# Kernel tuning notes

Measured on AMD Instinct MI355X. Metric: run time of the kernel, lower is better.

Reference implementation:

```python
import jax, jax.numpy as jnp
import numpy as np

B_SZ = 4; L = 2048; IN_DIM = 32; D_MODEL = 256; N_LAYERS = 2
ED = 512; N_STATE = 16; DT_RANK = 16; D_CONV = 4


def setup_inputs() -> dict:
    key = jax.random.key(0)
    ks = jax.random.split(key, 12)
    def rn(k, shape, scale=0.02):
        return jax.random.normal(k, shape, jnp.float32) * scale
    return {
        "x": jax.random.normal(ks[0], (B_SZ, L, IN_DIM), jnp.float32),
        "enc_w": rn(ks[1], (D_MODEL, IN_DIM), 0.1),
        "enc_b": jnp.zeros((D_MODEL,), jnp.float32),
        "norm_w": jnp.ones((N_LAYERS, D_MODEL), jnp.float32),
        "in_proj_w": rn(ks[2], (N_LAYERS, 2 * ED, D_MODEL)),
        "conv_w": rn(ks[3], (N_LAYERS, ED, D_CONV), 0.1),
        "conv_b": jnp.zeros((N_LAYERS, ED), jnp.float32),
        "x_proj_w": rn(ks[4], (N_LAYERS, DT_RANK + 2 * N_STATE, ED)),
        "dt_proj_w": rn(ks[5], (N_LAYERS, ED, DT_RANK), 0.1),
        "dt_proj_b": rn(ks[6], (N_LAYERS, ED), 0.5),
        # S4D-real init: A_log[l, e, n] = log(n+1)
        "A_log": jnp.log(jnp.tile(jnp.arange(1, N_STATE + 1, dtype=jnp.float32), (N_LAYERS, ED, 1))),
        "D_param": jnp.ones((N_LAYERS, ED), jnp.float32),
        "out_proj_w": rn(ks[7], (N_LAYERS, D_MODEL, ED)),
        "dec_w": rn(ks[8], (1, D_MODEL), 0.1),
        "dec_b": jnp.zeros((1,), jnp.float32),
    }


def _rmsnorm(x, w, eps=1e-5):
    return x * jax.lax.rsqrt(jnp.mean(x * x, axis=-1, keepdims=True) + eps) * w


def _silu(x):
    return x * jax.nn.sigmoid(x)


def _selective_scan(x, delta, A, Bm, Cm, Dp):
    # x, delta: (B, L, ED); A: (ED, N); Bm, Cm: (B, L, N); Dp: (ED,)
    def step(h, t):
        d_t, b_t, c_t, x_t = t  # (B,ED) (B,N) (B,N) (B,ED)
        dA = jnp.exp(d_t[..., None] * A)               # (B, ED, N)
        h = dA * h + (d_t * x_t)[..., None] * b_t[:, None, :]
        y = jnp.einsum('ben,bn->be', h, c_t)
        return h, y
    h0 = jnp.zeros((x.shape[0], A.shape[0], A.shape[1]), x.dtype)
    xs = (jnp.swapaxes(delta, 0, 1), jnp.swapaxes(Bm, 0, 1),
          jnp.swapaxes(Cm, 0, 1), jnp.swapaxes(x, 0, 1))
    _, ys = jax.lax.scan(step, h0, xs)                 # ys: (L, B, ED)
    return jnp.swapaxes(ys, 0, 1) + Dp * x


def _mamba_block(x, p):
    xz = jnp.einsum('bld,ed->ble', x, p['in_proj_w'])  # (B, L, 2*ED)
    xb, z = jnp.split(xz, 2, axis=-1)
    # causal depthwise conv over time
    xc = jnp.swapaxes(xb, 1, 2)                        # (B, ED, L)
    kern = p['conv_w'][:, None, :]                     # (ED, 1, K)
    xc = jax.lax.conv_general_dilated(xc, kern, (1,), [(D_CONV - 1, 0)],
                                      feature_group_count=ED)
    xb = _silu(jnp.swapaxes(xc, 1, 2) + p['conv_b'])
    dbc = jnp.einsum('ble,fe->blf', xb, p['x_proj_w'])
    dt, Bm, Cm = jnp.split(dbc, [DT_RANK, DT_RANK + N_STATE], axis=-1)
    delta = jax.nn.softplus(jnp.einsum('blr,er->ble', dt, p['dt_proj_w']) + p['dt_proj_b'])
    A = -jnp.exp(p['A_log'])
    y = _selective_scan(xb, delta, A, Bm, Cm, p['D_param'])
    y = y * _silu(z)
    return jnp.einsum('ble,de->bld', y, p['out_proj_w'])


def reference(x, enc_w, enc_b, norm_w, in_proj_w, conv_w, conv_b, x_proj_w,
              dt_proj_w, dt_proj_b, A_log, D_param, out_proj_w, dec_w, dec_b):
    h = jnp.einsum('bli,di->bld', x, enc_w) + enc_b
    for l in range(N_LAYERS):
        p = {'in_proj_w': in_proj_w[l], 'conv_w': conv_w[l], 'conv_b': conv_b[l],
             'x_proj_w': x_proj_w[l], 'dt_proj_w': dt_proj_w[l], 'dt_proj_b': dt_proj_b[l],
             'A_log': A_log[l], 'D_param': D_param[l], 'out_proj_w': out_proj_w[l]}
        h = h + _mamba_block(_rmsnorm(h, norm_w[l]), p)
    out = jax.nn.sigmoid(jnp.einsum('bld,od->blo', h, dec_w) + dec_b)
    return out[:, -1, 0]
```

## Files before the change

kernel.cpp:

```cpp
#include <hip/hip_runtime.h>
#include <math.h>

#define BSZ 4
#define SEQ 2048
#define INDIM 32
#define DM 256
#define ED 512
#define NST 16
#define DTR 16
#define MROWS (BSZ * SEQ)
#define CH 64
#define LC (SEQ / CH)

typedef unsigned short u16;
typedef unsigned int u32;
typedef __bf16 bf16x8 __attribute__((ext_vector_type(8)));
typedef float f32x4 __attribute__((ext_vector_type(4)));

__device__ __forceinline__ float silu_f(float x) { return x / (1.f + __expf(-x)); }

__device__ __forceinline__ u16 f2bf(float x) {
  union { float f; unsigned u; } c; c.f = x;
  return (u16)((c.u + 0x7FFF + ((c.u >> 16) & 1)) >> 16);
}
__device__ __forceinline__ float bf2f(u16 v) {
  union { unsigned u; float f; } c; c.u = ((unsigned)v) << 16;
  return c.f;
}
__device__ __forceinline__ u32 pack2(float lo, float hi) {
  return (u32)f2bf(lo) | ((u32)f2bf(hi) << 16);
}

template <bool ACCUM>
__global__ __launch_bounds__(256) void gemm_bf16_f32(const u16* __restrict__ A,
                                                     const u16* __restrict__ B,
                                                     float* __restrict__ C,
                                                     int M, int N, int K,
                                                     int lda, int ldc) {
  __shared__ u16 As[128][40];
  __shared__ u16 Bs[128][40];
  const int tid = threadIdx.x;
  const int m0 = blockIdx.y * 128;
  const int n0 = blockIdx.x * 128;
  const int wid = tid >> 6;
  const int lane = tid & 63;
  const int wm = (wid >> 1) * 64, wn = (wid & 1) * 64;
  const int l15 = lane & 15, l4 = lane >> 4;
  const int arow = tid >> 1;
  const int ak = (tid & 1) * 16;
  f32x4 acc[4][4];
  const f32x4 zero = {0.f, 0.f, 0.f, 0.f};
#pragma unroll
  for (int i = 0; i < 4; i++)
#pragma unroll
    for (int j = 0; j < 4; j++) acc[i][j] = zero;

  for (int k0 = 0; k0 < K; k0 += 32) {
    const u16* ap = A + (size_t)(m0 + arow) * lda + k0 + ak;
    *(int4*)&As[arow][ak]     = *(const int4*)(ap);
    *(int4*)&As[arow][ak + 8] = *(const int4*)(ap + 8);
    int4 bv0 = {0, 0, 0, 0}, bv1 = {0, 0, 0, 0};
    if (n0 + arow < N) {
      const u16* bp = B + (size_t)(n0 + arow) * K + k0 + ak;
      bv0 = *(const int4*)(bp);
      bv1 = *(const int4*)(bp + 8);
    }
    *(int4*)&Bs[arow][ak]     = bv0;
    *(int4*)&Bs[arow][ak + 8] = bv1;
    __syncthreads();
    bf16x8 af[4], bfr[4];
#pragma unroll
    for (int i = 0; i < 4; i++) {
      af[i]  = *(const bf16x8*)&As[wm + i * 16 + l15][l4 * 8];
      bfr[i] = *(const bf16x8*)&Bs[wn + i * 16 + l15][l4 * 8];
    }
#pragma unroll
    for (int i = 0; i < 4; i++)
#pragma unroll
      for (int j = 0; j < 4; j++)
        acc[i][j] = __builtin_amdgcn_mfma_f32_16x16x32_bf16(af[i], bfr[j], acc[i][j], 0, 0, 0);
    __syncthreads();
  }
#pragma unroll
  for (int i = 0; i < 4; i++) {
    const int mb = m0 + wm + i * 16 + l4 * 4;
#pragma unroll
    for (int j = 0; j < 4; j++) {
      const int n = n0 + wn + j * 16 + l15;
      if (n < N) {
        float* p = C + (size_t)mb * ldc + n;
#pragma unroll
        for (int r = 0; r < 4; r++) {
          float v = acc[i][j][r];
          if (ACCUM) v += p[(size_t)r * ldc];
          p[(size_t)r * ldc] = v;
        }
      }
    }
  }
}

__global__ __launch_bounds__(256) void gemm_bf16_u16(const u16* __restrict__ A,
                                                     const u16* __restrict__ B,
                                                     u16* __restrict__ C,
                                                     int M, int N, int K,
                                                     int lda, int ldc) {
  __shared__ u16 As[128][40];
  __shared__ u16 Bs[128][40];
  const int tid = threadIdx.x;
  const int m0 = blockIdx.y * 128;
  const int n0 = blockIdx.x * 128;
  const int wid = tid >> 6;
  const int lane = tid & 63;
  const int wm = (wid >> 1) * 64, wn = (wid & 1) * 64;
  const int l15 = lane & 15, l4 = lane >> 4;
  const int arow = tid >> 1;
  const int ak = (tid & 1) * 16;
  f32x4 acc[4][4];
  const f32x4 zero = {0.f, 0.f, 0.f, 0.f};
#pragma unroll
  for (int i = 0; i < 4; i++)
#pragma unroll
    for (int j = 0; j < 4; j++) acc[i][j] = zero;

  for (int k0 = 0; k0 < K; k0 += 32) {
    const u16* ap = A + (size_t)(m0 + arow) * lda + k0 + ak;
    *(int4*)&As[arow][ak]     = *(const int4*)(ap);
    *(int4*)&As[arow][ak + 8] = *(const int4*)(ap + 8);
    const u16* bp = B + (size_t)(n0 + arow) * K + k0 + ak;
    *(int4*)&Bs[arow][ak]     = *(const int4*)(bp);
    *(int4*)&Bs[arow][ak + 8] = *(const int4*)(bp + 8);
    __syncthreads();
    bf16x8 af[4], bfr[4];
#pragma unroll
    for (int i = 0; i < 4; i++) {
      af[i]  = *(const bf16x8*)&As[wm + i * 16 + l15][l4 * 8];
      bfr[i] = *(const bf16x8*)&Bs[wn + i * 16 + l15][l4 * 8];
    }
#pragma unroll
    for (int i = 0; i < 4; i++)
#pragma unroll
      for (int j = 0; j < 4; j++)
        acc[i][j] = __builtin_amdgcn_mfma_f32_16x16x32_bf16(af[i], bfr[j], acc[i][j], 0, 0, 0);
    __syncthreads();
  }
#pragma unroll
  for (int i = 0; i < 4; i++) {
    const int mb = m0 + wm + i * 16 + l4 * 4;
#pragma unroll
    for (int j = 0; j < 4; j++) {
      const int n = n0 + wn + j * 16 + l15;
      u16* p = C + (size_t)mb * ldc + n;
#pragma unroll
      for (int r = 0; r < 4; r++) p[(size_t)r * ldc] = f2bf(acc[i][j][r]);
    }
  }
}

__global__ __launch_bounds__(256) void gemm_nt_enc(const float* __restrict__ A,
                                                   const float* __restrict__ B,
                                                   const float* __restrict__ bias,
                                                   float* __restrict__ C,
                                                   int M, int N, int K, int lda) {
  __shared__ float As[16][65];
  __shared__ float Bs[16][65];
  const int tid = threadIdx.x;
  const int m0 = blockIdx.y * 64;
  const int n0 = blockIdx.x * 64;
  const int tm = tid & 15, tn = tid >> 4;
  const int lrow = tid >> 2;
  const int lk = (tid & 3) << 2;
  float acc[4][4] = {};
  for (int k0 = 0; k0 < K; k0 += 16) {
    {
      const float4 a = *(const float4*)(A + (size_t)(m0 + lrow) * lda + k0 + lk);
      As[lk + 0][lrow] = a.x; As[lk + 1][lrow] = a.y;
      As[lk + 2][lrow] = a.z; As[lk + 3][lrow] = a.w;
    }
    {
      float4 b = make_float4(0.f, 0.f, 0.f, 0.f);
      if (n0 + lrow < N) b = *(const float4*)(B + (size_t)(n0 + lrow) * K + k0 + lk);
      Bs[lk + 0][lrow] = b.x; Bs[lk + 1][lrow] = b.y;
      Bs[lk + 2][lrow] = b.z; Bs[lk + 3][lrow] = b.w;
    }
    __syncthreads();
#pragma unroll
    for (int k = 0; k < 16; k++) {
      float a4[4], b4[4];
#pragma unroll
      for (int i = 0; i < 4; i++) a4[i] = As[k][tm * 4 + i];
#pragma unroll
      for (int j = 0; j < 4; j++) b4[j] = Bs[k][tn * 4 + j];
#pragma unroll
      for (int i = 0; i < 4; i++)
#pragma unroll
        for (int j = 0; j < 4; j++) acc[i][j] = fmaf(a4[i], b4[j], acc[i][j]);
    }
    __syncthreads();
  }
#pragma unroll
  for (int i = 0; i < 4; i++) {
    const int m = m0 + tm * 4 + i;
#pragma unroll
    for (int j = 0; j < 4; j++) {
      const int n = n0 + tn * 4 + j;
      if (n < N) C[(size_t)m * N + n] = acc[i][j] + bias[n];
    }
  }
}

#define S_IN (2 * 1024 * 256)
#define S_OUT (2 * 256 * 512)
#define S_XP (2 * 48 * 512)
__global__ __launch_bounds__(256) void cvt_weights_k(const float* __restrict__ w1,
                                                     const float* __restrict__ w2,
                                                     const float* __restrict__ w3,
                                                     u16* __restrict__ o1,
                                                     u16* __restrict__ o2,
                                                     u16* __restrict__ o3) {
  const int i = blockIdx.x * 256 + threadIdx.x;
  if (i < S_IN) o1[i] = f2bf(w1[i]);
  else if (i < S_IN + S_OUT) o2[i - S_IN] = f2bf(w2[i - S_IN]);
  else if (i < S_IN + S_OUT + S_XP) o3[i - S_IN - S_OUT] = f2bf(w3[i - S_IN - S_OUT]);
}

__global__ __launch_bounds__(256) void rmsnorm_k(const float* __restrict__ h,
                                                 const float* __restrict__ w,
                                                 u16* __restrict__ out16) {
  __shared__ float sh[4];
  __shared__ float sscale;
  const int row = blockIdx.x;
  const int tid = threadIdx.x;
  const float v = h[(size_t)row * DM + tid];
  float s = v * v;
#pragma unroll
  for (int off = 32; off; off >>= 1) s += __shfl_xor(s, off, 64);
  if ((tid & 63) == 0) sh[tid >> 6] = s;
  __syncthreads();
  if (tid == 0) {
    float t = sh[0] + sh[1] + sh[2] + sh[3];
    sscale = rsqrtf(t * (1.0f / DM) + 1e-5f);
  }
  __syncthreads();
  out16[(size_t)row * DM + tid] = f2bf(v * sscale * w[tid]);
}

__global__ __launch_bounds__(256) void conv_silu_k(const u16* __restrict__ xz16,
                                                   const float* __restrict__ cw,
                                                   const float* __restrict__ cb,
                                                   u16* __restrict__ out16) {
  const int idx = blockIdx.x * 256 + threadIdx.x;
  const int e = idx & (ED - 1);
  const int row = idx >> 9;
  const int t = row & (SEQ - 1);
  const float4 w = *(const float4*)(cw + e * 4);
  const u16* col = xz16 + e;
  float acc = cb[e];
  const float v0 = (t >= 3) ? bf2f(col[(size_t)(row - 3) * 1024]) : 0.f;
  const float v1 = (t >= 2) ? bf2f(col[(size_t)(row - 2) * 1024]) : 0.f;
  const float v2 = (t >= 1) ? bf2f(col[(size_t)(row - 1) * 1024]) : 0.f;
  const float v3 = bf2f(col[(size_t)row * 1024]);
  acc += v0 * w.x + v1 * w.y + v2 * w.z + v3 * w.w;
  out16[idx] = f2bf(silu_f(acc));
}

__global__ __launch_bounds__(256) void dt_softplus_k(const float* __restrict__ dbc,
                                                     const float* __restrict__ dtw,
                                                     const float* __restrict__ dtb,
                                                     const u16* __restrict__ xbc16,
                                                     u32* __restrict__ pairs) {
  __shared__ float sdt[DTR];
  const int row = blockIdx.y;
  const int e = blockIdx.x * 256 + threadIdx.x;
  if (threadIdx.x < DTR) sdt[threadIdx.x] = dbc[(size_t)row * 48 + threadIdx.x];
  __syncthreads();
  const float* w = dtw + (size_t)e * DTR;
  float s = dtb[e];
#pragma unroll
  for (int r = 0; r < DTR; r++) s = fmaf(sdt[r], w[r], s);
  const float sp = fmaxf(s, 0.f) + log1pf(__expf(-fabsf(s)));
  const float xv = bf2f(xbc16[(size_t)row * ED + e]);
  pairs[(size_t)row * ED + e] = pack2(sp, sp * xv);
}

__global__ __launch_bounds__(256) void scan_pass1(const u32* __restrict__ pairs,
                                                  const float* __restrict__ dbc,
                                                  u16* __restrict__ hend16,
                                                  float* __restrict__ Sbuf,
                                                  const float* __restrict__ A_log) {
  __shared__ float sB[LC][16];
  const int tid = threadIdx.x;
  const int e = blockIdx.x * 256 + tid;
  const int c = blockIdx.y;
  const int b = blockIdx.z;
  const int row0 = b * SEQ + c * LC;
  float Aen[16];
  {
    const float4* ap = (const float4*)(A_log + (size_t)e * 16);
#pragma unroll
    for (int q = 0; q < 4; q++) {
      float4 v = ap[q];
      Aen[4 * q + 0] = -__expf(v.x); Aen[4 * q + 1] = -__expf(v.y);
      Aen[4 * q + 2] = -__expf(v.z); Aen[4 * q + 3] = -__expf(v.w);
    }
  }
  for (int idx = tid; idx < LC * 16; idx += 256)
    sB[idx >> 4][idx & 15] = dbc[(size_t)(row0 + (idx >> 4)) * 48 + DTR + (idx & 15)];
  __syncthreads();
  const u32* pp = pairs + (size_t)row0 * ED + e;
  float h[16];
#pragma unroll
  for (int n = 0; n < 16; n++) h[n] = 0.f;
  float S = 0.f;
  u32 p = pp[0];
  for (int t = 0; t < LC; t++) {
    const u32 pn = (t + 1 < LC) ? pp[(size_t)(t + 1) * ED] : p;
    const float d = bf2f((u16)(p & 0xffff));
    const float dx = bf2f((u16)(p >> 16));
    S += d;
    const float4* bp = (const float4*)sB[t];
    const float4 B0 = bp[0], B1 = bp[1], B2 = bp[2], B3 = bp[3];
    const float Bv[16] = {B0.x, B0.y, B0.z, B0.w, B1.x, B1.y, B1.z, B1.w,
                          B2.x, B2.y, B2.z, B2.w, B3.x, B3.y, B3.z, B3.w};
#pragma unroll
    for (int n = 0; n < 16; n++) h[n] = __expf(d * Aen[n]) * h[n] + dx * Bv[n];
    p = pn;
  }
  u32 wbuf[8];
#pragma unroll
  for (int q = 0; q < 8; q++) wbuf[q] = pack2(h[2 * q], h[2 * q + 1]);
  u16* hp = hend16 + ((size_t)(c * BSZ + b) * ED + e) * 16;
  *(int4*)(hp) = *(int4*)&wbuf[0];
  *(int4*)(hp + 8) = *(int4*)&wbuf[4];
  Sbuf[(size_t)(c * BSZ + b) * ED + e] = S;
}

__global__ __launch_bounds__(256) void scan_mid(u16* __restrict__ hend16,
                                                const float* __restrict__ Sbuf,
                                                const float* __restrict__ A_log) {
  const int idx = blockIdx.x * 256 + threadIdx.x;
  const int en = idx & 8191;
  const int b = idx >> 13;
  const int e = en >> 4;
  const float A = -__expf(A_log[en]);
  float h = 0.f;
#pragma unroll 4
  for (int c = 0; c < CH; c++) {
    const size_t base = (size_t)(c * BSZ + b) * 8192 + en;
    const float he = bf2f(hend16[base]);
    const float Sv = Sbuf[(size_t)(c * BSZ + b) * ED + e];
    hend16[base] = f2bf(h);
    h = __expf(A * Sv) * h + he;
  }
}

__global__ __launch_bounds__(256) void scan_pass2(const u32* __restrict__ pairs,
                                                  const u16* __restrict__ xbc16,
                                                  const float* __restrict__ dbc,
                                                  u16* __restrict__ xz16,
                                                  const u16* __restrict__ hin16,
                                                  const float* __restrict__ A_log,
                                                  const float* __restrict__ Dp) {
  __shared__ float sB[LC][16];
  __shared__ float sC[LC][16];
  const int tid = threadIdx.x;
  const int e = blockIdx.x * 256 + tid;
  const int c = blockIdx.y;
  const int b = blockIdx.z;
  const int row0 = b * SEQ + c * LC;
  float Aen[16];
  {
    const float4* ap = (const float4*)(A_log + (size_t)e * 16);
#pragma unroll
    for (int q = 0; q < 4; q++) {
      float4 v = ap[q];
      Aen[4 * q + 0] = -__expf(v.x); Aen[4 * q + 1] = -__expf(v.y);
      Aen[4 * q + 2] = -__expf(v.z); Aen[4 * q + 3] = -__expf(v.w);
    }
  }
  for (int idx = tid; idx < LC * 32; idx += 256) {
    const int i = idx >> 5, jj = idx & 31;
    const float v = dbc[(size_t)(row0 + i) * 48 + DTR + jj];
    if (jj < 16) sB[i][jj] = v; else sC[i][jj - 16] = v;
  }
  __syncthreads();
  float h[16];
  {
    const u16* hp = hin16 + ((size_t)(c * BSZ + b) * ED + e) * 16;
    int4 v0 = *(const int4*)(hp);
    int4 v1 = *(const int4*)(hp + 8);
    const u32* wv = (const u32*)&v0;
    const u32* wv1 = (const u32*)&v1;
#pragma unroll
    for (int q = 0; q < 4; q++) {
      h[2 * q] = bf2f((u16)(wv[q] & 0xffff));
      h[2 * q + 1] = bf2f((u16)(wv[q] >> 16));
      h[8 + 2 * q] = bf2f((u16)(wv1[q] & 0xffff));
      h[8 + 2 * q + 1] = bf2f((u16)(wv1[q] >> 16));
    }
  }
  const float De = Dp[e];
  const u32* pp = pairs + (size_t)row0 * ED + e;
  const u16* xp = xbc16 + (size_t)row0 * ED + e;
  const u16* zp = xz16 + (size_t)row0 * 1024 + ED + e;
  u16* yw = xz16 + (size_t)row0 * 1024 + e;
  u32 p = pp[0];
  float xv = bf2f(xp[0]);
  float zv = bf2f(zp[0]);
  for (int t = 0; t < LC; t++) {
    const int tn = (t + 1 < LC) ? t + 1 : t;
    const u32 pn = pp[(size_t)tn * ED];
    const float xnx = bf2f(xp[(size_t)tn * ED]);
    const float znx = bf2f(zp[(size_t)tn * 1024]);
    const float d = bf2f((u16)(p & 0xffff));
    const float dx = bf2f((u16)(p >> 16));
    const float4* bp = (const float4*)sB[t];
    const float4 B0 = bp[0], B1 = bp[1], B2 = bp[2], B3 = bp[3];
    const float Bv[16] = {B0.x, B0.y, B0.z, B0.w, B1.x, B1.y, B1.z, B1.w,
                          B2.x, B2.y, B2.z, B2.w, B3.x, B3.y, B3.z, B3.w};
    const float4* cp = (const float4*)sC[t];
    const float4 C0 = cp[0], C1 = cp[1], C2 = cp[2], C3 = cp[3];
    const float Cv[16] = {C0.x, C0.y, C0.z, C0.w, C1.x, C1.y, C1.z, C1.w,
                          C2.x, C2.y, C2.z, C2.w, C3.x, C3.y, C3.z, C3.w};
    float y0 = 0.f, y1 = 0.f, y2 = 0.f, y3 = 0.f;
#pragma unroll
    for (int n = 0; n < 16; n++) {
      h[n] = __expf(d * Aen[n]) * h[n] + dx * Bv[n];
      if ((n & 3) == 0) y0 = fmaf(h[n], Cv[n], y0);
      else if ((n & 3) == 1) y1 = fmaf(h[n], Cv[n], y1);
      else if ((n & 3) == 2) y2 = fmaf(h[n], Cv[n], y2);
      else y3 = fmaf(h[n], Cv[n], y3);
    }
    float y = ((y0 + y1) + (y2 + y3)) + De * xv;
    y *= silu_f(zv);
    yw[(size_t)t * 1024] = f2bf(y);
    p = pn; xv = xnx; zv = znx;
  }
}

__global__ __launch_bounds__(64) void decode_k(const float* __restrict__ h,
                                               const float* __restrict__ dw,
                                               const float* __restrict__ db,
                                               float* __restrict__ out) {
  const int b = blockIdx.x;
  const int tid = threadIdx.x;
  const float* row = h + ((size_t)b * SEQ + SEQ - 1) * DM;
  float s = 0.f;
  for (int i = tid; i < DM; i += 64) s = fmaf(row[i], dw[i], s);
#pragma unroll
  for (int off = 32; off; off >>= 1) s += __shfl_xor(s, off, 64);
  if (tid == 0) out[b] = 1.f / (1.f + __expf(-(s + db[0])));
}

extern "C" void kernel_launch(void* const* d_in, const int* in_sizes, int n_in,
                              void* d_out, int out_size, void* d_ws, size_t ws_size,
                              hipStream_t stream) {
  const float* x         = (const float*)d_in[0];
  const float* enc_w     = (const float*)d_in[1];
  const float* enc_b     = (const float*)d_in[2];
  const float* norm_w    = (const float*)d_in[3];
  const float* in_proj_w = (const float*)d_in[4];
  const float* conv_w    = (const float*)d_in[5];
  const float* conv_b    = (const float*)d_in[6];
  const float* x_proj_w  = (const float*)d_in[7];
  const float* dt_proj_w = (const float*)d_in[8];
  const float* dt_proj_b = (const float*)d_in[9];
  const float* A_log     = (const float*)d_in[10];
  const float* D_param   = (const float*)d_in[11];
  const float* out_proj_w= (const float*)d_in[12];
  const float* dec_w     = (const float*)d_in[13];
  const float* dec_b     = (const float*)d_in[14];
  float* out = (float*)d_out;

  float* ws = (float*)d_ws;
  float* h       = ws;
  u16*   xz16    = (u16*)(ws + 2097152);
  u16*   xbc16   = (u16*)(ws + 6291456);
  u32*   pairs   = (u32*)(ws + 8388608);
  float* dbc     = ws + 12582912;
  u16*   hend16  = (u16*)(ws + 12976128);
  float* Sbuf    = ws + 14024704;
  u16*   w16in   = (u16*)(ws + 14155776);
  u16*   w16out  = (u16*)(ws + 14417920);
  u16*   w16xp   = (u16*)(ws + 14548992);
  u16*   normed16 = hend16;

  const dim3 blk(256);

  cvt_weights_k<<<(S_IN + S_OUT + S_XP + 255) / 256, blk, 0, stream>>>(
      in_proj_w, out_proj_w, x_proj_w, w16in, w16out, w16xp);

  gemm_nt_enc<<<dim3(DM / 64, MROWS / 64), blk, 0, stream>>>(
      x, enc_w, enc_b, h, MROWS, DM, INDIM, INDIM);

  for (int l = 0; l < 2; l++) {
    const float* Al = A_log + (size_t)l * ED * NST;
    rmsnorm_k<<<MROWS, 256, 0, stream>>>(h, norm_w + (size_t)l * DM, normed16);
    gemm_bf16_u16<<<dim3(1024 / 128, MROWS / 128), blk, 0, stream>>>(
        normed16, w16in + (size_t)l * 1024 * DM, xz16, MROWS, 1024, DM, DM, 1024);
    conv_silu_k<<<(MROWS * ED) / 256, blk, 0, stream>>>(
        xz16, conv_w + (size_t)l * ED * 4, conv_b + (size_t)l * ED, xbc16);
    gemm_bf16_f32<false><<<dim3(1, MROWS / 128), blk, 0, stream>>>(
        xbc16, w16xp + (size_t)l * 48 * ED, dbc, MROWS, 48, ED, ED, 48);
    dt_softplus_k<<<dim3(2, MROWS), blk, 0, stream>>>(
        dbc, dt_proj_w + (size_t)l * ED * DTR, dt_proj_b + (size_t)l * ED,
        xbc16, pairs);
    scan_pass1<<<dim3(ED / 256, CH, BSZ), blk, 0, stream>>>(
        pairs, dbc, hend16, Sbuf, Al);
    scan_mid<<<(BSZ * ED * NST) / 256, blk, 0, stream>>>(hend16, Sbuf, Al);
    scan_pass2<<<dim3(ED / 256, CH, BSZ), blk, 0, stream>>>(
        pairs, xbc16, dbc, xz16, hend16, Al, D_param + (size_t)l * ED);
    gemm_bf16_f32<true><<<dim3(DM / 128, MROWS / 128), blk, 0, stream>>>(
        xz16, w16out + (size_t)l * DM * ED, h, MROWS, DM, ED, 1024, DM);
  }

  decode_k<<<4, 64, 0, stream>>>(h, dec_w, dec_b, out);
}
```

Measured before the change: 394.8 us.

## Fold dt_proj into x_proj GEMM and fuse scan passes into cooperative kernel

Precomputes a combined weight (dt_proj_w @ x_proj_w[:16]) so that a single MFMA GEMM produces delta pre-activations directly, with bias, softplus and the delta*x product fused into its epilogue, plus the B/C columns. The separate x_proj GEMM and dt_softplus kernels go away. The three scan kernels (pass1, mid, pass2) become one cooperative kernel that uses grid syncs, and the per-chunk pairs are cached in shared memory for reuse in the second pass. The x_proj GEMM now computes 544 output columns instead of 48. The delta projection moves to bf16 precision and the combined weights are rounded once, and the cooperative launch requires all 512 blocks to be co-resident with about 36KB of shared memory each.

```diff
diff --git a/kernel.cpp b/kernel.cpp
--- a/kernel.cpp
+++ b/kernel.cpp
@@ -1,5 +1,8 @@
 #include <hip/hip_runtime.h>
+#include <hip/hip_cooperative_groups.h>
 #include <math.h>
+
+namespace cg = cooperative_groups;
 
 #define BSZ 4
 #define SEQ 2048
@@ -11,6 +14,7 @@
 #define MROWS (BSZ * SEQ)
 #define CH 64
 #define LC (SEQ / CH)
+#define WXPE_LSTRIDE (544 * 512)
 
 typedef unsigned short u16;
 typedef unsigned int u32;
@@ -153,6 +157,80 @@
       u16* p = C + (size_t)mb * ldc + n;
 #pragma unroll
       for (int r = 0; r < 4; r++) p[(size_t)r * ldc] = f2bf(acc[i][j][r]);
+    }
+  }
+}
+
+__global__ __launch_bounds__(256) void gemm_xproj(const u16* __restrict__ A,
+                                                  const u16* __restrict__ Bw,
+                                                  const float* __restrict__ dtb,
+                                                  u32* __restrict__ pairs,
+                                                  float* __restrict__ BCout) {
+  __shared__ u16 As[128][40];
+  __shared__ u16 Bs[128][40];
+  const int tid = threadIdx.x;
+  const int m0 = blockIdx.y * 128;
+  const int n0 = blockIdx.x * 128;
+  const int wid = tid >> 6;
+  const int lane = tid & 63;
+  const int wm = (wid >> 1) * 64, wn = (wid & 1) * 64;
+  const int l15 = lane & 15, l4 = lane >> 4;
+  const int arow = tid >> 1;
+  const int ak = (tid & 1) * 16;
+  f32x4 acc[4][4];
+  const f32x4 zero = {0.f, 0.f, 0.f, 0.f};
+#pragma unroll
+  for (int i = 0; i < 4; i++)
+#pragma unroll
+    for (int j = 0; j < 4; j++) acc[i][j] = zero;
+
+  for (int k0 = 0; k0 < ED; k0 += 32) {
+    const u16* ap = A + (size_t)(m0 + arow) * ED + k0 + ak;
+    *(int4*)&As[arow][ak]     = *(const int4*)(ap);
+    *(int4*)&As[arow][ak + 8] = *(const int4*)(ap + 8);
+    int4 bv0 = {0, 0, 0, 0}, bv1 = {0, 0, 0, 0};
+    if (n0 + arow < 544) {
+      const u16* bp = Bw + (size_t)(n0 + arow) * ED + k0 + ak;
+      bv0 = *(const int4*)(bp);
+      bv1 = *(const int4*)(bp + 8);
+    }
+    *(int4*)&Bs[arow][ak]     = bv0;
+    *(int4*)&Bs[arow][ak + 8] = bv1;
+    __syncthreads();
+    bf16x8 af[4], bfr[4];
+#pragma unroll
+    for (int i = 0; i < 4; i++) {
+      af[i]  = *(const bf16x8*)&As[wm + i * 16 + l15][l4 * 8];
+      bfr[i] = *(const bf16x8*)&Bs[wn + i * 16 + l15][l4 * 8];
+    }
+#pragma unroll
+    for (int i = 0; i < 4; i++)
+#pragma unroll
+      for (int j = 0; j < 4; j++)
+        acc[i][j] = __builtin_amdgcn_mfma_f32_16x16x32_bf16(af[i], bfr[j], acc[i][j], 0, 0, 0);
+    __syncthreads();
+  }
+#pragma unroll
+  for (int i = 0; i < 4; i++) {
+    const int mb = m0 + wm + i * 16 + l4 * 4;
+#pragma unroll
+    for (int j = 0; j < 4; j++) {
+      const int n = n0 + wn + j * 16 + l15;
+      if (n < 512) {
+        const float bias = dtb[n];
+#pragma unroll
+        for (int r = 0; r < 4; r++) {
+          const int row = mb + r;
+          const float v = acc[i][j][r] + bias;
+          const float sp = fmaxf(v, 0.f) + log1pf(__expf(-fabsf(v)));
+          const float xv = bf2f(A[(size_t)row * ED + n]);
+          pairs[(size_t)row * ED + n] = pack2(sp, sp * xv);
+        }
+      } else if (n < 544) {
+#pragma unroll
+        for (int r = 0; r < 4; r++)
+          BCout[(size_t)(mb + r) * 32 + (n - 512)] = acc[i][j][r];
+      }
     }
   }
 }
@@ -211,17 +289,39 @@
 
 #define S_IN (2 * 1024 * 256)
 #define S_OUT (2 * 256 * 512)
-#define S_XP (2 * 48 * 512)
+#define S_BC (2 * 32 * 512)
 __global__ __launch_bounds__(256) void cvt_weights_k(const float* __restrict__ w1,
                                                      const float* __restrict__ w2,
-                                                     const float* __restrict__ w3,
+                                                     const float* __restrict__ xpw,
                                                      u16* __restrict__ o1,
                                                      u16* __restrict__ o2,
-                                                     u16* __restrict__ o3) {
+                                                     u16* __restrict__ wxpe) {
   const int i = blockIdx.x * 256 + threadIdx.x;
   if (i < S_IN) o1[i] = f2bf(w1[i]);
   else if (i < S_IN + S_OUT) o2[i - S_IN] = f2bf(w2[i - S_IN]);
-  else if (i < S_IN + S_OUT + S_XP) o3[i - S_IN - S_OUT] = f2bf(w3[i - S_IN - S_OUT]);
+  else if (i < S_IN + S_OUT + S_BC) {
+    const int i2 = i - S_IN - S_OUT;
+    const int l = i2 >> 14;
+    const int r = (i2 >> 9) & 31;
+    const int k = i2 & 511;
+    wxpe[(size_t)l * WXPE_LSTRIDE + (512 + r) * 512 + k] =
+        f2bf(xpw[(size_t)l * 48 * 512 + (16 + r) * 512 + k]);
+  }
+}
+
+__global__ __launch_bounds__(256) void wcomb_k(const float* __restrict__ dtw,
+                                               const float* __restrict__ xpw,
+                                               u16* __restrict__ wxpe) {
+  const int i = blockIdx.x * 256 + threadIdx.x;
+  const int l = i >> 18;
+  const int e = (i >> 9) & 511;
+  const int k = i & 511;
+  const float* dw = dtw + ((size_t)l * 512 + e) * 16;
+  const float* xw = xpw + (size_t)l * 48 * 512 + k;
+  float s = 0.f;
+#pragma unroll
+  for (int r = 0; r < 16; r++) s = fmaf(dw[r], xw[(size_t)r * 512], s);
+  wxpe[(size_t)l * WXPE_LSTRIDE + (size_t)e * 512 + k] = f2bf(s);
 }
 
 __global__ __launch_bounds__(256) void rmsnorm_k(const float* __restrict__ h,
@@ -264,35 +364,23 @@
   out16[idx] = f2bf(silu_f(acc));
 }
 
-__global__ __launch_bounds__(256) void dt_softplus_k(const float* __restrict__ dbc,
-                                                     const float* __restrict__ dtw,
-                                                     const float* __restrict__ dtb,
-                                                     const u16* __restrict__ xbc16,
-                                                     u32* __restrict__ pairs) {
-  __shared__ float sdt[DTR];
-  const int row = blockIdx.y;
-  const int e = blockIdx.x * 256 + threadIdx.x;
-  if (threadIdx.x < DTR) sdt[threadIdx.x] = dbc[(size_t)row * 48 + threadIdx.x];
-  __syncthreads();
-  const float* w = dtw + (size_t)e * DTR;
-  float s = dtb[e];
-#pragma unroll
-  for (int r = 0; r < DTR; r++) s = fmaf(sdt[r], w[r], s);
-  const float sp = fmaxf(s, 0.f) + log1pf(__expf(-fabsf(s)));
-  const float xv = bf2f(xbc16[(size_t)row * ED + e]);
-  pairs[(size_t)row * ED + e] = pack2(sp, sp * xv);
-}
-
-__global__ __launch_bounds__(256) void scan_pass1(const u32* __restrict__ pairs,
-                                                  const float* __restrict__ dbc,
-                                                  u16* __restrict__ hend16,
-                                                  float* __restrict__ Sbuf,
-                                                  const float* __restrict__ A_log) {
+__global__ __launch_bounds__(256) void scan_coop(const u32* __restrict__ pairs,
+                                                 const u16* __restrict__ xbc16,
+                                                 const float* __restrict__ BC,
+                                                 u16* __restrict__ xz16,
+                                                 u16* __restrict__ hbuf,
+                                                 float* __restrict__ Sbuf,
+                                                 const float* __restrict__ A_log,
+                                                 const float* __restrict__ Dp) {
+  __shared__ u32 sP[LC][256];
   __shared__ float sB[LC][16];
-  const int tid = threadIdx.x;
-  const int e = blockIdx.x * 256 + tid;
-  const int c = blockIdx.y;
-  const int b = blockIdx.z;
+  __shared__ float sC[LC][16];
+  const int tid = threadIdx.x;
+  const int blk = blockIdx.x;
+  const int x = blk & 1;
+  const int c = (blk >> 1) & (CH - 1);
+  const int b = blk >> 7;
+  const int e = x * 256 + tid;
   const int row0 = b * SEQ + c * LC;
   float Aen[16];
   {
@@ -304,89 +392,66 @@
       Aen[4 * q + 2] = -__expf(v.z); Aen[4 * q + 3] = -__expf(v.w);
     }
   }
-  for (int idx = tid; idx < LC * 16; idx += 256)
-    sB[idx >> 4][idx & 15] = dbc[(size_t)(row0 + (idx >> 4)) * 48 + DTR + (idx & 15)];
-  __syncthreads();
-  const u32* pp = pairs + (size_t)row0 * ED + e;
-  float h[16];
-#pragma unroll
-  for (int n = 0; n < 16; n++) h[n] = 0.f;
-  float S = 0.f;
-  u32 p = pp[0];
-  for (int t = 0; t < LC; t++) {
-    const u32 pn = (t + 1 < LC) ? pp[(size_t)(t + 1) * ED] : p;
-    const float d = bf2f((u16)(p & 0xffff));
-    const float dx = bf2f((u16)(p >> 16));
-    S += d;
-    const float4* bp = (const float4*)sB[t];
-    const float4 B0 = bp[0], B1 = bp[1], B2 = bp[2], B3 = bp[3];
-    const float Bv[16] = {B0.x, B0.y, B0.z, B0.w, B1.x, B1.y, B1.z, B1.w,
-                          B2.x, B2.y, B2.z, B2.w, B3.x, B3.y, B3.z, B3.w};
-#pragma unroll
-    for (int n = 0; n < 16; n++) h[n] = __expf(d * Aen[n]) * h[n] + dx * Bv[n];
-    p = pn;
-  }
-  u32 wbuf[8];
-#pragma unroll
-  for (int q = 0; q < 8; q++) wbuf[q] = pack2(h[2 * q], h[2 * q + 1]);
-  u16* hp = hend16 + ((size_t)(c * BSZ + b) * ED + e) * 16;
-  *(int4*)(hp) = *(int4*)&wbuf[0];
-  *(int4*)(hp + 8) = *(int4*)&wbuf[4];
-  Sbuf[(size_t)(c * BSZ + b) * ED + e] = S;
-}
-
-__global__ __launch_bounds__(256) void scan_mid(u16* __restrict__ hend16,
-                                                const float* __restrict__ Sbuf,
-                                                const float* __restrict__ A_log) {
-  const int idx = blockIdx.x * 256 + threadIdx.x;
-  const int en = idx & 8191;
-  const int b = idx >> 13;
-  const int e = en >> 4;
-  const float A = -__expf(A_log[en]);
-  float h = 0.f;
-#pragma unroll 4
-  for (int c = 0; c < CH; c++) {
-    const size_t base = (size_t)(c * BSZ + b) * 8192 + en;
-    const float he = bf2f(hend16[base]);
-    const float Sv = Sbuf[(size_t)(c * BSZ + b) * ED + e];
-    hend16[base] = f2bf(h);
-    h = __expf(A * Sv) * h + he;
-  }
-}
-
-__global__ __launch_bounds__(256) void scan_pass2(const u32* __restrict__ pairs,
-                                                  const u16* __restrict__ xbc16,
-                                                  const float* __restrict__ dbc,
-                                                  u16* __restrict__ xz16,
-                                                  const u16* __restrict__ hin16,
-                                                  const float* __restrict__ A_log,
-                                                  const float* __restrict__ Dp) {
-  __shared__ float sB[LC][16];
-  __shared__ float sC[LC][16];
-  const int tid = threadIdx.x;
-  const int e = blockIdx.x * 256 + tid;
-  const int c = blockIdx.y;
-  const int b = blockIdx.z;
-  const int row0 = b * SEQ + c * LC;
-  float Aen[16];
-  {
-    const float4* ap = (const float4*)(A_log + (size_t)e * 16);
-#pragma unroll
-    for (int q = 0; q < 4; q++) {
-      float4 v = ap[q];
-      Aen[4 * q + 0] = -__expf(v.x); Aen[4 * q + 1] = -__expf(v.y);
-      Aen[4 * q + 2] = -__expf(v.z); Aen[4 * q + 3] = -__expf(v.w);
-    }
-  }
   for (int idx = tid; idx < LC * 32; idx += 256) {
     const int i = idx >> 5, jj = idx & 31;
-    const float v = dbc[(size_t)(row0 + i) * 48 + DTR + jj];
+    const float v = BC[(size_t)(row0 + i) * 32 + jj];
     if (jj < 16) sB[i][jj] = v; else sC[i][jj - 16] = v;
   }
   __syncthreads();
-  float h[16];
   {
-    const u16* hp = hin16 + ((size_t)(c * BSZ + b) * ED + e) * 16;
+    const u32* pp = pairs + (size_t)row0 * ED + e;
+    float h[16];
+#pragma unroll
+    for (int n = 0; n < 16; n++) h[n] = 0.f;
+    float S = 0.f;
+    u32 p = pp[0];
+    for (int t = 0; t < LC; t++) {
+      const u32 pn = (t + 1 < LC) ? pp[(size_t)(t + 1) * ED] : p;
+      sP[t][tid] = p;
+      const float d = bf2f((u16)(p & 0xffff));
+      const float dx = bf2f((u16)(p >> 16));
+      S += d;
+      const float4* bp = (const float4*)sB[t];
+      const float4 B0 = bp[0], B1 = bp[1], B2 = bp[2], B3 = bp[3];
+      const float Bv[16] = {B0.x, B0.y, B0.z, B0.w, B1.x, B1.y, B1.z, B1.w,
+                            B2.x, B2.y, B2.z, B2.w, B3.x, B3.y, B3.z, B3.w};
+#pragma unroll
+      for (int n = 0; n < 16; n++) h[n] = __expf(d * Aen[n]) * h[n] + dx * Bv[n];
+      p = pn;
+    }
+    u32 wbuf[8];
+#pragma unroll
+    for (int q = 0; q < 8; q++) wbuf[q] = pack2(h[2 * q], h[2 * q + 1]);
+    u16* hp = hbuf + ((size_t)(c * BSZ + b) * ED + e) * 16;
+    *(int4*)(hp) = *(int4*)&wbuf[0];
+    *(int4*)(hp + 8) = *(int4*)&wbuf[4];
+    Sbuf[(size_t)(c * BSZ + b) * ED + e] = S;
+  }
+  __threadfence();
+  cg::this_grid().sync();
+  {
+    const int gid = blk * 256 + tid;
+    if (gid < BSZ * ED * NST) {
+      const int en = gid & 8191;
+      const int bb = gid >> 13;
+      const int ee = en >> 4;
+      const float A = -__expf(A_log[en]);
+      float hh = 0.f;
+#pragma unroll 4
+      for (int cc = 0; cc < CH; cc++) {
+        const size_t base = (size_t)(cc * BSZ + bb) * 8192 + en;
+        const float he = bf2f(hbuf[base]);
+        const float Sv = Sbuf[(size_t)(cc * BSZ + bb) * ED + ee];
+        hbuf[base] = f2bf(hh);
+        hh = __expf(A * Sv) * hh + he;
+      }
+    }
+  }
+  __threadfence();
+  cg::this_grid().sync();
+  {
+    float h[16];
+    const u16* hp = hbuf + ((size_t)(c * BSZ + b) * ED + e) * 16;
     int4 v0 = *(const int4*)(hp);
     int4 v1 = *(const int4*)(hp + 8);
     const u32* wv = (const u32*)&v0;
@@ -398,43 +463,41 @@
       h[8 + 2 * q] = bf2f((u16)(wv1[q] & 0xffff));
       h[8 + 2 * q + 1] = bf2f((u16)(wv1[q] >> 16));
     }
-  }
-  const float De = Dp[e];
-  const u32* pp = pairs + (size_t)row0 * ED + e;
-  const u16* xp = xbc16 + (size_t)row0 * ED + e;
-  const u16* zp = xz16 + (size_t)row0 * 1024 + ED + e;
-  u16* yw = xz16 + (size_t)row0 * 1024 + e;
-  u32 p = pp[0];
-  float xv = bf2f(xp[0]);
-  float zv = bf2f(zp[0]);
-  for (int t = 0; t < LC; t++) {
-    const int tn = (t + 1 < LC) ? t + 1 : t;
-    const u32 pn = pp[(size_t)tn * ED];
-    const float xnx = bf2f(xp[(size_t)tn * ED]);
-    const float znx = bf2f(zp[(size_t)tn * 1024]);
-    const float d = bf2f((u16)(p & 0xffff));
-    const float dx = bf2f((u16)(p >> 16));
-    const float4* bp = (const float4*)sB[t];
-    const float4 B0 = bp[0], B1 = bp[1], B2 = bp[2], B3 = bp[3];
-    const float Bv[16] = {B0.x, B0.y, B0.z, B0.w, B1.x, B1.y, B1.z, B1.w,
-                          B2.x, B2.y, B2.z, B2.w, B3.x, B3.y, B3.z, B3.w};
-    const float4* cp = (const float4*)sC[t];
-    const float4 C0 = cp[0], C1 = cp[1], C2 = cp[2], C3 = cp[3];
-    const float Cv[16] = {C0.x, C0.y, C0.z, C0.w, C1.x, C1.y, C1.z, C1.w,
-                          C2.x, C2.y, C2.z, C2.w, C3.x, C3.y, C3.z, C3.w};
-    float y0 = 0.f, y1 = 0.f, y2 = 0.f, y3 = 0.f;
-#pragma unroll
-    for (int n = 0; n < 16; n++) {
-      h[n] = __expf(d * Aen[n]) * h[n] + dx * Bv[n];
-      if ((n & 3) == 0) y0 = fmaf(h[n], Cv[n], y0);
-      else if ((n & 3) == 1) y1 = fmaf(h[n], Cv[n], y1);
-      else if ((n & 3) == 2) y2 = fmaf(h[n], Cv[n], y2);
-      else y3 = fmaf(h[n], Cv[n], y3);
-    }
-    float y = ((y0 + y1) + (y2 + y3)) + De * xv;
-    y *= silu_f(zv);
-    yw[(size_t)t * 1024] = f2bf(y);
-    p = pn; xv = xnx; zv = znx;
+    const float De = Dp[e];
+    const u16* xp = xbc16 + (size_t)row0 * ED + e;
+    const u16* zp = xz16 + (size_t)row0 * 1024 + ED + e;
+    u16* yw = xz16 + (size_t)row0 * 1024 + e;
+    float xv = bf2f(xp[0]);
+    float zv = bf2f(zp[0]);
+    for (int t = 0; t < LC; t++) {
+      const int tn = (t + 1 < LC) ? t + 1 : t;
+      const float xnx = bf2f(xp[(size_t)tn * ED]);
+      const float znx = bf2f(zp[(size_t)tn * 1024]);
+      const u32 p = sP[t][tid];
+      const float d = bf2f((u16)(p & 0xffff));
+      const float dx = bf2f((u16)(p >> 16));
+      const float4* bp = (const float4*)sB[t];
+      const float4 B0 = bp[0], B1 = bp[1], B2 = bp[2], B3 = bp[3];
+      const float Bv[16] = {B0.x, B0.y, B0.z, B0.w, B1.x, B1.y, B1.z, B1.w,
+                            B2.x, B2.y, B2.z, B2.w, B3.x, B3.y, B3.z, B3.w};
+      const float4* cp = (const float4*)sC[t];
+      const float4 C0 = cp[0], C1 = cp[1], C2 = cp[2], C3 = cp[3];
+      const float Cv[16] = {C0.x, C0.y, C0.z, C0.w, C1.x, C1.y, C1.z, C1.w,
+                            C2.x, C2.y, C2.z, C2.w, C3.x, C3.y, C3.z, C3.w};
+      float y0 = 0.f, y1 = 0.f, y2 = 0.f, y3 = 0.f;
+#pragma unroll
+      for (int n = 0; n < 16; n++) {
+        h[n] = __expf(d * Aen[n]) * h[n] + dx * Bv[n];
+        if ((n & 3) == 0) y0 = fmaf(h[n], Cv[n], y0);
+        else if ((n & 3) == 1) y1 = fmaf(h[n], Cv[n], y1);
+        else if ((n & 3) == 2) y2 = fmaf(h[n], Cv[n], y2);
+        else y3 = fmaf(h[n], Cv[n], y3);
+      }
+      float y = ((y0 + y1) + (y2 + y3)) + De * xv;
+      y *= silu_f(zv);
+      yw[(size_t)t * 1024] = f2bf(y);
+      xv = xnx; zv = znx;
+    }
   }
 }
 
@@ -476,40 +539,43 @@
   float* h       = ws;
   u16*   xz16    = (u16*)(ws + 2097152);
   u16*   xbc16   = (u16*)(ws + 6291456);
-  u32*   pairs   = (u32*)(ws + 8388608);
-  float* dbc     = ws + 12582912;
-  u16*   hend16  = (u16*)(ws + 12976128);
-  float* Sbuf    = ws + 14024704;
-  u16*   w16in   = (u16*)(ws + 14155776);
-  u16*   w16out  = (u16*)(ws + 14417920);
-  u16*   w16xp   = (u16*)(ws + 14548992);
-  u16*   normed16 = hend16;
+  u32*   pairs   = (u32*)(ws + 7340032);
+  float* BC      = ws + 11534336;
+  u16*   hbuf    = (u16*)(ws + 11796480);
+  float* Sbuf    = ws + 12845056;
+  u16*   w16in   = (u16*)(ws + 12976128);
+  u16*   w16out  = (u16*)(ws + 13238272);
+  u16*   wxpe    = (u16*)(ws + 13369344);
+  u16*   normed16 = hbuf;
 
   const dim3 blk(256);
 
-  cvt_weights_k<<<(S_IN + S_OUT + S_XP + 255) / 256, blk, 0, stream>>>(
-      in_proj_w, out_proj_w, x_proj_w, w16in, w16out, w16xp);
+  cvt_weights_k<<<(S_IN + S_OUT + S_BC + 255) / 256, blk, 0, stream>>>(
+      in_proj_w, out_proj_w, x_proj_w, w16in, w16out, wxpe);
+  wcomb_k<<<(2 * 512 * 512) / 256, blk, 0, stream>>>(dt_proj_w, x_proj_w, wxpe);
 
   gemm_nt_enc<<<dim3(DM / 64, MROWS / 64), blk, 0, stream>>>(
       x, enc_w, enc_b, h, MROWS, DM, INDIM, INDIM);
 
   for (int l = 0; l < 2; l++) {
     const float* Al = A_log + (size_t)l * ED * NST;
+    const float* Dl = D_param + (size_t)l * ED;
     rmsnorm_k<<<MROWS, 256, 0, stream>>>(h, norm_w + (size_t)l * DM, normed16);
     gemm_bf16_u16<<<dim3(1024 / 128, MROWS / 128), blk, 0, stream>>>(
         normed16, w16in + (size_t)l * 1024 * DM, xz16, MROWS, 1024, DM, DM, 1024);
     conv_silu_k<<<(MROWS * ED) / 256, blk, 0, stream>>>(
         xz16, conv_w + (size_t)l * ED * 4, conv_b + (size_t)l * ED, xbc16);
-    gemm_bf16_f32<false><<<dim3(1, MROWS / 128), blk, 0, stream>>>(
-        xbc16, w16xp + (size_t)l * 48 * ED, dbc, MROWS, 48, ED, ED, 48);
-    dt_softplus_k<<<dim3(2, MROWS), blk, 0, stream>>>(
-        dbc, dt_proj_w + (size_t)l * ED * DTR, dt_proj_b + (size_t)l * ED,
-        xbc16, pairs);
-    scan_pass1<<<dim3(ED / 256, CH, BSZ), blk, 0, stream>>>(
-        pairs, dbc, hend16, Sbuf, Al);
-    scan_mid<<<(BSZ * ED * NST) / 256, blk, 0, stream>>>(hend16, Sbuf, Al);
-    scan_pass2<<<dim3(ED / 256, CH, BSZ), blk, 0, stream>>>(
-        pairs, xbc16, dbc, xz16, hend16, Al, D_param + (size_t)l * ED);
+    gemm_xproj<<<dim3(5, MROWS / 128), blk, 0, stream>>>(
+        xbc16, wxpe + (size_t)l * WXPE_LSTRIDE, dt_proj_b + (size_t)l * ED,
+        pairs, BC);
+    {
+      const u32* a0 = pairs; const u16* a1 = xbc16; const float* a2 = BC;
+      u16* a3 = xz16; u16* a4 = hbuf; float* a5 = Sbuf;
+      const float* a6 = Al; const float* a7 = Dl;
+      void* args[] = {&a0, &a1, &a2, &a3, &a4, &a5, &a6, &a7};
+      hipLaunchCooperativeKernel((void*)scan_coop, dim3(512), dim3(256),
+                                 args, 0, stream);
+    }
     gemm_bf16_f32<true><<<dim3(DM / 128, MROWS / 128), blk, 0, stream>>>(
         xz16, w16out + (size_t)l * DM * ED, h, MROWS, DM, ED, 1024, DM);
   }
```

Result: slower. 857.6 us (+117.2%).
